# Kernel optimization log

Measured on AMD Instinct MI355X. Metric: run time of the kernel, lower is better.

Reference implementation:

```python
import jax, jax.numpy as jnp
import numpy as np

N = 4096
DIMS = {"word": 768, "pos": 64, "liwc": 93, "entity": 256, "text": 768}
HID, OUT = 256, 128
VIEWS = ["word", "pos", "liwc", "entity", "text"]


def setup_inputs() -> dict:
    key = jax.random.key(0)
    inp = {}
    for i, v in enumerate(VIEWS):
        ka, kx, k1, k2 = jax.random.split(jax.random.fold_in(key, i), 4)
        d = DIMS[v]
        # dense row-normalized adjacency surrogate
        a = jax.random.uniform(ka, (N, N), dtype=jnp.float32)
        inp[f"adj_{v}"] = a / jnp.sum(a, axis=1, keepdims=True)
        inp[f"x_{v}"] = jax.random.normal(kx, (N, d), dtype=jnp.float32)
        inp[f"W1_{v}"] = jax.random.normal(k1, (d, HID), dtype=jnp.float32) * (2.0 / (d + HID)) ** 0.5
        inp[f"b1_{v}"] = jnp.zeros((HID,), dtype=jnp.float32)
        inp[f"W2_{v}"] = jax.random.normal(k2, (HID, OUT), dtype=jnp.float32) * (2.0 / (HID + OUT)) ** 0.5
        inp[f"b2_{v}"] = jnp.zeros((OUT,), dtype=jnp.float32)
    return inp


def _gcn2(adj, x, W1, b1, W2, b2):
    # layer 1: adj @ (x @ W1) + b1, relu (dropout is identity in eval mode)
    h = jax.nn.relu(adj @ (x @ W1) + b1)
    # layer 2
    return adj @ (h @ W2) + b2


def reference(adj_word, adj_pos, adj_liwc, adj_entity, adj_text,
              x_word, x_pos, x_liwc, x_entity, x_text,
              W1_word, b1_word, W2_word, b2_word,
              W1_pos, b1_pos, W2_pos, b2_pos,
              W1_liwc, b1_liwc, W2_liwc, b2_liwc,
              W1_entity, b1_entity, W2_entity, b2_entity,
              W1_text, b1_text, W2_text, b2_text):
    return (
        _gcn2(adj_word, x_word, W1_word, b1_word, W2_word, b2_word),
        _gcn2(adj_pos, x_pos, W1_pos, b1_pos, W2_pos, b2_pos),
        _gcn2(adj_liwc, x_liwc, W1_liwc, b1_liwc, W2_liwc, b2_liwc),
        _gcn2(adj_entity, x_entity, W1_entity, b1_entity, W2_entity, b2_entity),
        _gcn2(adj_text, x_text, W1_text, b1_text, W2_text, b2_text),
    )
```

## Files before the change

### kernel.cpp

```cpp
#include <hip/hip_runtime.h>
#include <stdint.h>

typedef unsigned short u16;
typedef __attribute__((ext_vector_type(8))) __bf16 bf16x8;
typedef __attribute__((ext_vector_type(4))) float f32x4;
typedef __attribute__((ext_vector_type(4))) u16 u16x4;
typedef __attribute__((ext_vector_type(8))) u16 u16x8;

#define BM 128
#define BN 128
#define BK 32
#define MTOT 4096

__device__ __forceinline__ u16 f2bf(float f) {
  union { float f; uint32_t u; } x; x.f = f;
  uint32_t r = x.u + 0x7FFFu + ((x.u >> 16) & 1u);
  return (u16)(r >> 16);
}
__device__ __forceinline__ float bf2f(u16 h) {
  union { uint32_t u; float f; } x; x.u = ((uint32_t)h) << 16;
  return x.f;
}

__device__ __forceinline__ void gload16(const void* g, void* lds) {
  __builtin_amdgcn_global_load_lds(
      (const __attribute__((address_space(1))) void*)g,
      (__attribute__((address_space(3))) void*)lds, 16, 0, 0);
}

struct ViewParams {
  const void* A;
  const u16* BT;
  void* C;
  const float* bias;
  int ldab, lda, N;
  int kspan;
  size_t partStride;
};
struct Params5 { ViewParams v[5]; };

template <int FLAGS, bool AF32, bool CF32>
__global__ __launch_bounds__(256) void gemm_kernel(Params5 p, int tilesPerView,
                                                   int ntiles, int kchunks) {
  constexpr int ABYTES = AF32 ? (BM * BK * 4) : (BM * BK * 2);
  __shared__ __align__(16) char smem[ABYTES + BN * BK * 2];
  u16* Bs = (u16*)(smem + ABYTES);

  const int bid = blockIdx.x;
  const int view = bid / tilesPerView;
  const int t = bid - view * tilesPerView;
  const int kc = t % kchunks;
  const int t2 = t / kchunks;
  const int nt = t2 % ntiles;
  const int mt = t2 / ntiles;
  ViewParams vp = p.v[view];
  const int ldab = vp.ldab, lda = vp.lda, N = vp.N;
  const int m0 = mt * BM, n0 = nt * BN;
  const int kbase = kc * vp.kspan;

  const int tid = threadIdx.x;
  const int wave = tid >> 6;
  const int lane = tid & 63;

  const int srow = lane >> 2;
  const int slot4 = lane & 3;
  const int rB0 = wave * 32 + srow;
  const int rB1 = rB0 + 16;
  const int cB0 = slot4 ^ ((rB0 >> 1) & 3);
  const int cB1 = slot4 ^ ((rB1 >> 1) & 3);
  const u16* gB0 = vp.BT + (size_t)(n0 + rB0) * ldab + kbase + cB0 * 8;
  const u16* gB1 = vp.BT + (size_t)(n0 + rB1) * ldab + kbase + cB1 * 8;
  u16* lB0 = Bs + (wave * 32) * 32;
  u16* lB1 = Bs + (wave * 32 + 16) * 32;

  const float* gAf[4];
  float* lAf[4];
  const u16 *gAb0 = nullptr, *gAb1 = nullptr;
  u16 *lAb0 = nullptr, *lAb1 = nullptr;
  if constexpr (AF32) {
    const float* Af = (const float*)vp.A;
    const int arow = lane >> 3;
    const int slot8 = lane & 7;
#pragma unroll
    for (int i = 0; i < 4; i++) {
      int r = wave * 32 + i * 8 + arow;
      int c = slot8 ^ (r & 7);
      gAf[i] = Af + (size_t)(m0 + r) * lda + kbase + c * 4;
      lAf[i] = (float*)smem + (wave * 32 + i * 8) * 32;
    }
  } else {
    const u16* Ab = (const u16*)vp.A;
    const int rA0 = wave * 32 + srow;
    const int rA1 = rA0 + 16;
    const int cA0 = slot4 ^ ((rA0 >> 1) & 3);
    const int cA1 = slot4 ^ ((rA1 >> 1) & 3);
    gAb0 = Ab + (size_t)(m0 + rA0) * lda + kbase + cA0 * 8;
    gAb1 = Ab + (size_t)(m0 + rA1) * lda + kbase + cA1 * 8;
    lAb0 = (u16*)smem + (wave * 32) * 32;
    lAb1 = (u16*)smem + (wave * 32 + 16) * 32;
  }

  const int lm = lane & 15;
  const int q = lane >> 4;
  const int wm = (wave >> 1) * 64;
  const int wn = (wave & 1) * 64;
  int aoff0[4], aoff1[4], boff[4];
#pragma unroll
  for (int i = 0; i < 4; i++) {
    int ml = wm + i * 16 + lm;
    if constexpr (AF32) {
      aoff0[i] = ml * 32 + ((2 * q) ^ (ml & 7)) * 4;
      aoff1[i] = ml * 32 + ((2 * q + 1) ^ (ml & 7)) * 4;
    } else {
      aoff0[i] = ml * 32 + (q ^ ((ml >> 1) & 3)) * 8;
    }
    int nl = wn + i * 16 + lm;
    boff[i] = nl * 32 + (q ^ ((nl >> 1) & 3)) * 8;
  }

  f32x4 acc[4][4];
#pragma unroll
  for (int i = 0; i < 4; i++)
#pragma unroll
    for (int j = 0; j < 4; j++) acc[i][j] = 0.0f;

  for (int ks = 0; ks < vp.kspan; ks += BK) {
    if constexpr (AF32) {
#pragma unroll
      for (int i = 0; i < 4; i++) { gload16(gAf[i], lAf[i]); gAf[i] += BK; }
    } else {
      gload16(gAb0, lAb0); gload16(gAb1, lAb1);
      gAb0 += BK; gAb1 += BK;
    }
    gload16(gB0, lB0); gload16(gB1, lB1);
    gB0 += BK; gB1 += BK;
    __syncthreads();

    bf16x8 af[4], bfr[4];
#pragma unroll
    for (int i = 0; i < 4; i++) {
      if constexpr (AF32) {
        f32x4 lo = *(const f32x4*)((const float*)smem + aoff0[i]);
        f32x4 hi = *(const f32x4*)((const float*)smem + aoff1[i]);
        bf16x8 a;
#pragma unroll
        for (int tt = 0; tt < 4; tt++) { a[tt] = (__bf16)lo[tt]; a[tt + 4] = (__bf16)hi[tt]; }
        af[i] = a;
      } else {
        af[i] = *(const bf16x8*)((const u16*)smem + aoff0[i]);
      }
    }
#pragma unroll
    for (int j = 0; j < 4; j++) bfr[j] = *(const bf16x8*)(Bs + boff[j]);
#pragma unroll
    for (int i = 0; i < 4; i++)
#pragma unroll
      for (int j = 0; j < 4; j++)
        acc[i][j] = __builtin_amdgcn_mfma_f32_16x16x32_bf16(af[i], bfr[j], acc[i][j], 0, 0, 0);
    __syncthreads();
  }

#pragma unroll
  for (int j = 0; j < 4; j++) {
    const int n = n0 + wn + j * 16 + lm;
    float bv = 0.0f;
    if (FLAGS & 2) bv = vp.bias[n];
#pragma unroll
    for (int i = 0; i < 4; i++) {
      const int mb = m0 + wm + i * 16 + q * 4;
      float v0 = acc[i][j][0], v1 = acc[i][j][1], v2 = acc[i][j][2], v3 = acc[i][j][3];
      if (FLAGS & 2) { v0 += bv; v1 += bv; v2 += bv; v3 += bv; }
      if (FLAGS & 4) {
        v0 = fmaxf(v0, 0.0f); v1 = fmaxf(v1, 0.0f);
        v2 = fmaxf(v2, 0.0f); v3 = fmaxf(v3, 0.0f);
      }
      if constexpr ((FLAGS & 1) != 0) {
        u16x4 pk;
        pk[0] = f2bf(v0); pk[1] = f2bf(v1); pk[2] = f2bf(v2); pk[3] = f2bf(v3);
        *(u16x4*)((u16*)vp.C + (size_t)kc * vp.partStride + (size_t)n * MTOT + mb) = pk;
      } else if constexpr (CF32) {
        float* cp = (float*)vp.C + (size_t)mb * N + n;
        cp[0] = v0; cp[N] = v1; cp[2 * N] = v2; cp[3 * N] = v3;
      } else {
        u16* cp = (u16*)vp.C + (size_t)kc * vp.partStride + (size_t)mb * N + n;
        cp[0] = f2bf(v0); cp[N] = f2bf(v1); cp[2 * N] = f2bf(v2); cp[3 * N] = f2bf(v3);
      }
    }
  }
}

struct CvtParams { const float* src[5]; u16* dst; };
__global__ __launch_bounds__(256) void cvt_kernel(CvtParams cp) {
  long i = (long)blockIdx.x * 256 + threadIdx.x;
  int v = (int)(i >> 21);
  long r = i & ((1L << 21) - 1);
  const f32x4* p = (const f32x4*)cp.src[v] + r * 2;
  f32x4 a = p[0], b = p[1];
  u16x8 o;
#pragma unroll
  for (int t = 0; t < 4; t++) { o[t] = f2bf(a[t]); o[t + 4] = f2bf(b[t]); }
  ((u16x8*)cp.dst)[i] = o;
}

struct CombParams { const u16* parts; u16* out; const float* b[5]; int kchunks; };
template <bool RELU>
__global__ __launch_bounds__(256) void comb_kernel(CombParams cp) {
  int idx = blockIdx.x * 256 + threadIdx.x;
  int v = idx >> 17;
  int e = (idx & 131071) << 3;
  float acc[8] = {0, 0, 0, 0, 0, 0, 0, 0};
  for (int kc = 0; kc < cp.kchunks; kc++) {
    u16x8 t = *(const u16x8*)(cp.parts + (((size_t)(kc * 5 + v)) << 20) + e);
#pragma unroll
    for (int j = 0; j < 8; j++) acc[j] += bf2f(t[j]);
  }
  if (RELU) {
    float bv = cp.b[v][e >> 12];
#pragma unroll
    for (int j = 0; j < 8; j++) acc[j] = fmaxf(acc[j] + bv, 0.0f);
  }
  u16x8 o;
#pragma unroll
  for (int j = 0; j < 8; j++) o[j] = f2bf(acc[j]);
  *(u16x8*)(cp.out + (((size_t)v) << 20) + e) = o;
}

struct PrepParams {
  const float* W1[5]; u16* W1T[5];
  const float* W2[5]; u16* W2T[5];
  const float* xl; float* xlp;
  int d[5]; int Kp[5];
};

__global__ void prep_kernel(PrepParams p, int total) {
  int idx = blockIdx.x * 256 + threadIdx.x;
  if (idx >= total) return;
  int off = 0;
#pragma unroll
  for (int v = 0; v < 5; v++) {
    int sz = 256 * p.Kp[v];
    if (idx < off + sz) {
      int r = idx - off;
      int n = r / p.Kp[v];
      int k = r - n * p.Kp[v];
      p.W1T[v][r] = (k < p.d[v]) ? f2bf(p.W1[v][(size_t)k * 256 + n]) : (u16)0;
      return;
    }
    off += sz;
  }
#pragma unroll
  for (int v = 0; v < 5; v++) {
    if (idx < off + 128 * 256) {
      int r = idx - off;
      int n = r >> 8, k = r & 255;
      p.W2T[v][r] = f2bf(p.W2[v][(size_t)k * 128 + n]);
      return;
    }
    off += 128 * 256;
  }
  {
    int r = idx - off;
    int m = r / 96, k = r - m * 96;
    p.xlp[r] = (k < 93) ? p.xl[(size_t)m * 93 + k] : 0.0f;
  }
}

extern "C" void kernel_launch(void* const* d_in, const int* in_sizes, int n_in,
                              void* d_out, int out_size, void* d_ws, size_t ws_size,
                              hipStream_t stream) {
  (void)in_sizes; (void)n_in; (void)out_size;
  static const int dims[5] = {768, 64, 93, 256, 768};
  static const int Kp[5]   = {768, 64, 96, 256, 768};

  const float *adjf[5], *xf[5], *W1f[5], *b1f[5], *W2f[5], *b2f[5];
  for (int v = 0; v < 5; v++) {
    adjf[v] = (const float*)d_in[6 * v + 0];
    xf[v]   = (const float*)d_in[6 * v + 1];
    W1f[v]  = (const float*)d_in[6 * v + 2];
    b1f[v]  = (const float*)d_in[6 * v + 3];
    W2f[v]  = (const float*)d_in[6 * v + 4];
    b2f[v]  = (const float*)d_in[6 * v + 5];
  }

  const size_t VIEW = (size_t)256 * 4096;
  char* ws = (char*)d_ws;
  size_t off = 0;
  auto carve = [&](size_t bytes) { char* pp = ws + off; off += (bytes + 15) & ~(size_t)15; return pp; };
  u16* W1T[5]; for (int v = 0; v < 5; v++) W1T[v] = (u16*)carve((size_t)256 * Kp[v] * 2);
  u16* W2T[5]; for (int v = 0; v < 5; v++) W2T[v] = (u16*)carve((size_t)128 * 256 * 2);
  float* xlp = (float*)carve((size_t)4096 * 96 * 4);
  u16* Y1T = (u16*)carve(5 * VIEW * 2);
  u16* PARTS = (u16*)carve(2 * 5 * VIEW * 2);
  u16* HT = (u16*)carve(5 * VIEW * 2);
  u16* adjb = (u16*)carve((size_t)5 * 4096 * 4096 * 2);
  const bool ksplit = ws_size >= off;
  u16* G = Y1T;

  PrepParams pp;
  int prepTot = 0;
  for (int v = 0; v < 5; v++) {
    pp.W1[v] = W1f[v]; pp.W1T[v] = W1T[v];
    pp.W2[v] = W2f[v]; pp.W2T[v] = W2T[v];
    pp.d[v] = dims[v]; pp.Kp[v] = Kp[v];
    prepTot += 256 * Kp[v];
  }
  pp.xl = xf[2]; pp.xlp = xlp;
  prepTot += 5 * 128 * 256 + 4096 * 96;
  prep_kernel<<<(prepTot + 255) / 256, 256, 0, stream>>>(pp, prepTot);

  Params5 pa;
  for (int v = 0; v < 5; v++)
    pa.v[v] = ViewParams{ (v == 2 ? (const void*)xlp : (const void*)xf[v]), W1T[v], Y1T + v * VIEW,
                          nullptr, Kp[v], Kp[v], 256, Kp[v], 0 };
  gemm_kernel<1, true, false><<<320, 256, 0, stream>>>(pa, 64, 2, 1);

  CvtParams cv;
  for (int v = 0; v < 5; v++) cv.src[v] = adjf[v];
  cv.dst = adjb;
  cvt_kernel<<<40960, 256, 0, stream>>>(cv);

  if (ksplit) {
    Params5 pb;
    for (int v = 0; v < 5; v++)
      pb.v[v] = ViewParams{ adjb + (size_t)v * 4096 * 4096, Y1T + v * VIEW, PARTS + v * VIEW,
                            nullptr, 4096, 4096, 256, 2048, 5 * VIEW };
    gemm_kernel<1, false, false><<<640, 256, 0, stream>>>(pb, 128, 2, 2);

    CombParams c1{ PARTS, HT, { b1f[0], b1f[1], b1f[2], b1f[3], b1f[4] }, 2 };
    comb_kernel<true><<<2560, 256, 0, stream>>>(c1);

    Params5 pc;
    for (int v = 0; v < 5; v++)
      pc.v[v] = ViewParams{ adjb + (size_t)v * 4096 * 4096, HT + v * VIEW, PARTS + v * VIEW,
                            nullptr, 4096, 4096, 256, 2048, 5 * VIEW };
    gemm_kernel<0, false, false><<<640, 256, 0, stream>>>(pc, 128, 2, 2);

    CombParams c2{ PARTS, G, { nullptr, nullptr, nullptr, nullptr, nullptr }, 2 };
    comb_kernel<false><<<2560, 256, 0, stream>>>(c2);
  } else {
    Params5 pb;
    for (int v = 0; v < 5; v++)
      pb.v[v] = ViewParams{ adjb + (size_t)v * 4096 * 4096, Y1T + v * VIEW, HT + v * VIEW,
                            b1f[v], 4096, 4096, 256, 4096, 0 };
    gemm_kernel<7, false, false><<<320, 256, 0, stream>>>(pb, 64, 2, 1);
    Params5 pc;
    for (int v = 0; v < 5; v++)
      pc.v[v] = ViewParams{ adjb + (size_t)v * 4096 * 4096, HT + v * VIEW, G + v * VIEW,
                            nullptr, 4096, 4096, 256, 4096, 0 };
    gemm_kernel<0, false, false><<<320, 256, 0, stream>>>(pc, 64, 2, 1);
  }

  Params5 pd;
  float* outp = (float*)d_out;
  for (int v = 0; v < 5; v++)
    pd.v[v] = ViewParams{ G + v * VIEW, W2T[v], outp + (size_t)v * 4096 * 128, b2f[v],
                          256, 256, 128, 256, 0 };
  gemm_kernel<2, false, true><<<160, 256, 0, stream>>>(pd, 32, 1, 1);
}
```

Baseline: 612.0 us.

## Reassociate second GCN layer to multiply by W2 before the adjacency

The second layer now computes H@W2 first and then adj@(H@W2), rather than (adj@H)@W2. This halves the N in the big adjacency GEMM from 256 to 128 and writes fp32 split-K partials, which a new combine kernel sums with b2 straight into the output. The layer-1 epilogue and combine kernels are adjusted to match, and the adj conversion kernel is reshaped to four elements per thread. The intermediate T is rounded to bf16 before the large GEMM, which shifts where precision is lost.

```diff
diff --git a/kernel.cpp b/kernel.cpp
--- a/kernel.cpp
+++ b/kernel.cpp
@@ -179,7 +179,7 @@
         pk[0] = f2bf(v0); pk[1] = f2bf(v1); pk[2] = f2bf(v2); pk[3] = f2bf(v3);
         *(u16x4*)((u16*)vp.C + (size_t)kc * vp.partStride + (size_t)n * MTOT + mb) = pk;
       } else if constexpr (CF32) {
-        float* cp = (float*)vp.C + (size_t)mb * N + n;
+        float* cp = (float*)vp.C + (size_t)kc * vp.partStride + (size_t)mb * N + n;
         cp[0] = v0; cp[N] = v1; cp[2 * N] = v2; cp[3 * N] = v3;
       } else {
         u16* cp = (u16*)vp.C + (size_t)kc * vp.partStride + (size_t)mb * N + n;
@@ -192,19 +192,17 @@
 struct CvtParams { const float* src[5]; u16* dst; };
 __global__ __launch_bounds__(256) void cvt_kernel(CvtParams cp) {
   long i = (long)blockIdx.x * 256 + threadIdx.x;
-  int v = (int)(i >> 21);
-  long r = i & ((1L << 21) - 1);
-  const f32x4* p = (const f32x4*)cp.src[v] + r * 2;
-  f32x4 a = p[0], b = p[1];
-  u16x8 o;
-#pragma unroll
-  for (int t = 0; t < 4; t++) { o[t] = f2bf(a[t]); o[t + 4] = f2bf(b[t]); }
-  ((u16x8*)cp.dst)[i] = o;
+  int v = (int)(i >> 22);
+  long r = i & ((1L << 22) - 1);
+  f32x4 a = ((const f32x4*)cp.src[v])[r];
+  u16x4 o;
+#pragma unroll
+  for (int t = 0; t < 4; t++) o[t] = f2bf(a[t]);
+  ((u16x4*)cp.dst)[i] = o;
 }
 
 struct CombParams { const u16* parts; u16* out; const float* b[5]; int kchunks; };
-template <bool RELU>
-__global__ __launch_bounds__(256) void comb_kernel(CombParams cp) {
+__global__ __launch_bounds__(256) void comb_h_kernel(CombParams cp) {
   int idx = blockIdx.x * 256 + threadIdx.x;
   int v = idx >> 17;
   int e = (idx & 131071) << 3;
@@ -214,15 +212,33 @@
 #pragma unroll
     for (int j = 0; j < 8; j++) acc[j] += bf2f(t[j]);
   }
-  if (RELU) {
-    float bv = cp.b[v][e >> 12];
-#pragma unroll
-    for (int j = 0; j < 8; j++) acc[j] = fmaxf(acc[j] + bv, 0.0f);
-  }
+  const float* bp = cp.b[v] + (e & 255);
   u16x8 o;
 #pragma unroll
-  for (int j = 0; j < 8; j++) o[j] = f2bf(acc[j]);
+  for (int j = 0; j < 8; j++) o[j] = f2bf(fmaxf(acc[j] + bp[j], 0.0f));
   *(u16x8*)(cp.out + (((size_t)v) << 20) + e) = o;
+}
+
+struct CombFParams { const float* parts; float* out; const float* b[5]; int kchunks; };
+__global__ __launch_bounds__(256) void combf_kernel(CombFParams cp) {
+  int idx = blockIdx.x * 256 + threadIdx.x;
+  int v = idx >> 16;
+  int e = (idx & 65535) << 3;
+  float acc[8] = {0, 0, 0, 0, 0, 0, 0, 0};
+  for (int kc = 0; kc < cp.kchunks; kc++) {
+    const float* pp = cp.parts + (((size_t)(kc * 5 + v)) << 19) + e;
+    f32x4 a = *(const f32x4*)pp;
+    f32x4 b = *(const f32x4*)(pp + 4);
+#pragma unroll
+    for (int j = 0; j < 4; j++) { acc[j] += a[j]; acc[j + 4] += b[j]; }
+  }
+  const float* bp = cp.b[v] + (e & 127);
+  f32x4 o0, o1;
+#pragma unroll
+  for (int j = 0; j < 4; j++) { o0[j] = acc[j] + bp[j]; o1[j] = acc[j + 4] + bp[j + 4]; }
+  float* op = cp.out + (((size_t)v) << 19) + e;
+  *(f32x4*)op = o0;
+  *(f32x4*)(op + 4) = o1;
 }
 
 struct PrepParams {
@@ -283,6 +299,7 @@
   }
 
   const size_t VIEW = (size_t)256 * 4096;
+  const size_t TV   = (size_t)128 * 4096;
   char* ws = (char*)d_ws;
   size_t off = 0;
   auto carve = [&](size_t bytes) { char* pp = ws + off; off += (bytes + 15) & ~(size_t)15; return pp; };
@@ -294,7 +311,8 @@
   u16* HT = (u16*)carve(5 * VIEW * 2);
   u16* adjb = (u16*)carve((size_t)5 * 4096 * 4096 * 2);
   const bool ksplit = ws_size >= off;
-  u16* G = Y1T;
+  u16* TT = Y1T;
+  float* PARTSF = (float*)PARTS;
 
   PrepParams pp;
   int prepTot = 0;
@@ -317,43 +335,50 @@
   CvtParams cv;
   for (int v = 0; v < 5; v++) cv.src[v] = adjf[v];
   cv.dst = adjb;
-  cvt_kernel<<<40960, 256, 0, stream>>>(cv);
+  cvt_kernel<<<81920, 256, 0, stream>>>(cv);
 
   if (ksplit) {
     Params5 pb;
     for (int v = 0; v < 5; v++)
       pb.v[v] = ViewParams{ adjb + (size_t)v * 4096 * 4096, Y1T + v * VIEW, PARTS + v * VIEW,
                             nullptr, 4096, 4096, 256, 2048, 5 * VIEW };
-    gemm_kernel<1, false, false><<<640, 256, 0, stream>>>(pb, 128, 2, 2);
+    gemm_kernel<0, false, false><<<640, 256, 0, stream>>>(pb, 128, 2, 2);
 
     CombParams c1{ PARTS, HT, { b1f[0], b1f[1], b1f[2], b1f[3], b1f[4] }, 2 };
-    comb_kernel<true><<<2560, 256, 0, stream>>>(c1);
+    comb_h_kernel<<<2560, 256, 0, stream>>>(c1);
 
     Params5 pc;
     for (int v = 0; v < 5; v++)
-      pc.v[v] = ViewParams{ adjb + (size_t)v * 4096 * 4096, HT + v * VIEW, PARTS + v * VIEW,
-                            nullptr, 4096, 4096, 256, 2048, 5 * VIEW };
-    gemm_kernel<0, false, false><<<640, 256, 0, stream>>>(pc, 128, 2, 2);
-
-    CombParams c2{ PARTS, G, { nullptr, nullptr, nullptr, nullptr, nullptr }, 2 };
-    comb_kernel<false><<<2560, 256, 0, stream>>>(c2);
+      pc.v[v] = ViewParams{ HT + v * VIEW, W2T[v], TT + v * TV,
+                            nullptr, 256, 256, 128, 256, 0 };
+    gemm_kernel<1, false, false><<<160, 256, 0, stream>>>(pc, 32, 1, 1);
+
+    Params5 pd;
+    for (int v = 0; v < 5; v++)
+      pd.v[v] = ViewParams{ adjb + (size_t)v * 4096 * 4096, TT + v * TV, PARTSF + v * TV,
+                            nullptr, 4096, 4096, 128, 2048, 5 * TV };
+    gemm_kernel<0, false, true><<<320, 256, 0, stream>>>(pd, 64, 1, 2);
+
+    CombFParams c2{ PARTSF, (float*)d_out, { b2f[0], b2f[1], b2f[2], b2f[3], b2f[4] }, 2 };
+    combf_kernel<<<1280, 256, 0, stream>>>(c2);
   } else {
     Params5 pb;
     for (int v = 0; v < 5; v++)
       pb.v[v] = ViewParams{ adjb + (size_t)v * 4096 * 4096, Y1T + v * VIEW, HT + v * VIEW,
                             b1f[v], 4096, 4096, 256, 4096, 0 };
-    gemm_kernel<7, false, false><<<320, 256, 0, stream>>>(pb, 64, 2, 1);
+    gemm_kernel<6, false, false><<<320, 256, 0, stream>>>(pb, 64, 2, 1);
+
     Params5 pc;
     for (int v = 0; v < 5; v++)
-      pc.v[v] = ViewParams{ adjb + (size_t)v * 4096 * 4096, HT + v * VIEW, G + v * VIEW,
-                            nullptr, 4096, 4096, 256, 4096, 0 };
-    gemm_kernel<0, false, false><<<320, 256, 0, stream>>>(pc, 64, 2, 1);
-  }
-
-  Params5 pd;
-  float* outp = (float*)d_out;
-  for (int v = 0; v < 5; v++)
-    pd.v[v] = ViewParams{ G + v * VIEW, W2T[v], outp + (size_t)v * 4096 * 128, b2f[v],
-                          256, 256, 128, 256, 0 };
-  gemm_kernel<2, false, true><<<160, 256, 0, stream>>>(pd, 32, 1, 1);
-}
+      pc.v[v] = ViewParams{ HT + v * VIEW, W2T[v], TT + v * TV,
+                            nullptr, 256, 256, 128, 256, 0 };
+    gemm_kernel<1, false, false><<<160, 256, 0, stream>>>(pc, 32, 1, 1);
+
+    Params5 pd;
+    float* outp = (float*)d_out;
+    for (int v = 0; v < 5; v++)
+      pd.v[v] = ViewParams{ adjb + (size_t)v * 4096 * 4096, TT + v * TV, outp + v * TV,
+                            b2f[v], 4096, 4096, 128, 4096, 0 };
+    gemm_kernel<2, false, true><<<160, 256, 0, stream>>>(pd, 32, 1, 1);
+  }
+}
```

Measured after the change: 585.7 us. -4.3%, faster.
